# Kernel tuning notes

Measured on AMD Instinct MI355X. Metric: run time of the kernel, lower is better.

Reference implementation:

```python
import jax, jax.numpy as jnp
import numpy as np

NUM_USERS = 100000
NUM_ITEMS = 50000
N_NODES = NUM_USERS + NUM_ITEMS
N_EDGES = 2_000_000
D = 64          # embedding_dim
HEADS = 4
F1 = D // HEADS  # per-head out dim of gat1
BATCH = 16384
NEG_SLOPE = 0.2  # PyG GATConv default negative_slope


def setup_inputs() -> dict:
    key = jax.random.key(0)
    ks = jax.random.split(key, 13)
    inp = {}
    inp["edge_index"] = jax.random.randint(ks[0], (2, N_EDGES), 0, N_NODES, dtype=jnp.int64)
    inp["batch_user_idx"] = jax.random.randint(ks[1], (BATCH,), 0, NUM_USERS, dtype=jnp.int64)
    inp["batch_item_idx"] = jax.random.randint(ks[2], (BATCH,), 0, NUM_ITEMS, dtype=jnp.int64)
    # Embedding tables (nn.init.normal_ std=0.01)
    inp["user_emb"] = 0.01 * jax.random.normal(ks[3], (NUM_USERS, D), dtype=jnp.float32)
    inp["item_emb"] = 0.01 * jax.random.normal(ks[4], (NUM_ITEMS, D), dtype=jnp.float32)
    # gat1: GATConv(64, 16, heads=4, concat=True)
    inp["W1"] = jax.random.normal(ks[5], (D, HEADS * F1), dtype=jnp.float32) / np.sqrt(D)
    inp["a_src1"] = jax.random.normal(ks[6], (HEADS, F1), dtype=jnp.float32) / np.sqrt(F1)
    inp["a_dst1"] = jax.random.normal(ks[7], (HEADS, F1), dtype=jnp.float32) / np.sqrt(F1)
    inp["b1"] = jnp.zeros((HEADS * F1,), dtype=jnp.float32)
    # gat2: GATConv(64, 64, heads=1)
    inp["W2"] = jax.random.normal(ks[8], (D, D), dtype=jnp.float32) / np.sqrt(D)
    inp["a_src2"] = jax.random.normal(ks[9], (1, D), dtype=jnp.float32) / np.sqrt(D)
    inp["a_dst2"] = jax.random.normal(ks[10], (1, D), dtype=jnp.float32) / np.sqrt(D)
    inp["b2"] = jnp.zeros((D,), dtype=jnp.float32)
    return inp


def _gat_conv(x, src, dst, W, a_src, a_dst, b, num_nodes):
    """PyG GATConv (eval mode, concat, self-loops already in src/dst)."""
    H, F = a_src.shape
    h = (x @ W).reshape(num_nodes, H, F)                 # [N,H,F]
    alpha_s = jnp.einsum('nhf,hf->nh', h, a_src)         # [N,H]
    alpha_d = jnp.einsum('nhf,hf->nh', h, a_dst)
    e = alpha_s[src] + alpha_d[dst]                      # [E,H]
    e = jax.nn.leaky_relu(e, NEG_SLOPE)
    # scatter-softmax over destination neighborhoods
    m = jax.ops.segment_max(e, dst, num_segments=num_nodes)   # [N,H]
    e = jnp.exp(e - m[dst])
    denom = jax.ops.segment_sum(e, dst, num_segments=num_nodes)
    alpha = e / denom[dst]                               # [E,H]
    msg = h[src] * alpha[:, :, None]                     # [E,H,F]
    agg = jax.ops.segment_sum(msg, dst, num_segments=num_nodes)  # [N,H,F]
    return agg.reshape(num_nodes, H * F) + b


def reference(user_emb, item_emb, W1, a_src1, a_dst1, b1,
              W2, a_src2, a_dst2, b2,
              edge_index, batch_user_idx, batch_item_idx):
    x = jnp.concatenate([user_emb, item_emb], axis=0)    # [N,D]
    n = x.shape[0]
    loop = jnp.arange(n, dtype=edge_index.dtype)          # add_self_loops=True
    src = jnp.concatenate([edge_index[0], loop])
    dst = jnp.concatenate([edge_index[1], loop])
    x = jax.nn.elu(_gat_conv(x, src, dst, W1, a_src1, a_dst1, b1, n))
    x = jax.nn.elu(_gat_conv(x, src, dst, W2, a_src2, a_dst2, b2, n))
    u = x[batch_user_idx]
    v = x[batch_item_idx + NUM_USERS]
    return jax.nn.sigmoid(jnp.sum(u * v, axis=1))        # [BATCH]
```

## Files before the change

### kernel.cpp

```cpp
#include <hip/hip_runtime.h>
#include <math.h>

#define SHIFT 8
#define NBMAX 1024
#define CAP   4096
#define TILE  4096
#define HSCALE 64.0f

typedef float v2f __attribute__((ext_vector_type(2)));
typedef short bf16x8 __attribute__((ext_vector_type(8)));
typedef float f32x4 __attribute__((ext_vector_type(4)));

__device__ __forceinline__ unsigned short f2bf(float f) {
    unsigned u = __float_as_uint(f);
    unsigned r = u + 0x7FFFu + ((u >> 16) & 1u);
    return (unsigned short)(r >> 16);
}
__device__ __forceinline__ unsigned pack2bf(float lo, float hi) {
    return (unsigned)f2bf(lo) | ((unsigned)f2bf(hi) << 16);
}
__device__ __forceinline__ float bflo(unsigned u) { return __uint_as_float(u << 16); }
__device__ __forceinline__ float bfhi(unsigned u) { return __uint_as_float(u & 0xFFFF0000u); }


__global__ void k_prep_w(const float* __restrict__ W1, const float* __restrict__ W2,
                         unsigned short* __restrict__ WT1, unsigned short* __restrict__ WT2,
                         unsigned* __restrict__ gcur, int NB) {
    int t = blockIdx.x * 256 + threadIdx.x;
    if (t < 4096) {
        int n = t & 63, k = t >> 6;
        WT1[n * 64 + k] = f2bf(W1[k * 64 + n]);
        WT2[n * 64 + k] = f2bf(W2[k * 64 + n]);
    }
    if (t < NB) gcur[t] = (unsigned)t * CAP;
}


__global__ __launch_bounds__(512) void k_partition(
    const int* __restrict__ src, const int* __restrict__ dst, int E,
    unsigned* __restrict__ gcur, unsigned* __restrict__ pairs, int NB) {
    __shared__ unsigned lh[NBMAX];
    __shared__ unsigned lcur[NBMAX];
    int t = threadIdx.x;
    for (int q = t; q < NB; q += 512) lh[q] = 0;
    __syncthreads();
    int base = blockIdx.x * TILE;
    int end = min(E, base + TILE);
    for (int i = base + t; i < end; i += 512)
        atomicAdd(&lh[((unsigned)dst[i]) >> SHIFT], 1u);
    __syncthreads();
    for (int q = t; q < NB; q += 512) {
        unsigned c = lh[q];
        lcur[q] = c ? atomicAdd(&gcur[q], c) : 0u;
    }
    __syncthreads();
    for (int i = base + t; i < end; i += 512) {
        unsigned d = (unsigned)dst[i];
        unsigned pos = atomicAdd(&lcur[d >> SHIFT], 1u);
        pairs[pos] = ((d & 255u) << 18) | (unsigned)src[i];
    }
}

__global__ __launch_bounds__(512) void k_bucket_sort(
    const unsigned* __restrict__ pairs, const unsigned* __restrict__ gcur,
    unsigned* __restrict__ beg, unsigned* __restrict__ endd,
    int* __restrict__ srt, int N, int NB) {
    __shared__ unsigned lh[256];
    __shared__ unsigned lcur[256];
    __shared__ unsigned sh[256];
    __shared__ int ssrt[CAP];
    int b = blockIdx.x;
    int t = threadIdx.x;
    unsigned s0 = (unsigned)b * CAP;
    int cnt = (int)(gcur[b] - s0);
    if (t < 256) lh[t] = 0;
    __syncthreads();
    for (int i = t; i < cnt; i += 512)
        atomicAdd(&lh[pairs[s0 + i] >> 18], 1u);
    __syncthreads();
    unsigned deg_t = 0;
    if (t < 256) { deg_t = lh[t]; sh[t] = deg_t; }
    __syncthreads();
    for (int off = 1; off < 256; off <<= 1) {
        unsigned x = 0;
        if (t < 256 && t >= off) x = sh[t - off];
        __syncthreads();
        if (t < 256) sh[t] += x;
        __syncthreads();
    }
    if (t < 256) {
        unsigned excl = sh[t] - deg_t;
        lcur[t] = excl;
        int node = (b << SHIFT) + t;
        if (node < N) { beg[node] = s0 + excl; endd[node] = s0 + excl + deg_t; }
    }
    __syncthreads();
    for (int i = t; i < cnt; i += 512) {
        unsigned pk = pairs[s0 + i];
        unsigned p = atomicAdd(&lcur[pk >> 18], 1u);
        ssrt[p] = (int)(pk & 0x3FFFFu);
    }
    __syncthreads();
    for (int i = t; i < cnt; i += 512) srt[s0 + i] = ssrt[i];
}


template <int HT, int BIN>
__global__ __launch_bounds__(256) void k_linear_mfma(
    const void* __restrict__ xav, const void* __restrict__ xbv, int split,
    const unsigned short* __restrict__ WTg,
    const float* __restrict__ a_src, const float* __restrict__ a_dst,
    unsigned char* __restrict__ h, float* __restrict__ as_out,
    float* __restrict__ ad_out, int N) {
    __shared__ unsigned short sX[64 * 72];
    __shared__ unsigned short sWT[64 * 72];
    __shared__ float sH[64 * 68];
    int t = threadIdx.x;
    int nodeBase = blockIdx.x * 64;

    {
        int r = t >> 2, c4 = (t & 3) * 16;
        int n = nodeBase + r;
        uint4 A = {0,0,0,0}, Bv = {0,0,0,0};
        if (BIN) {
            if (n < N) {
                const unsigned short* row = (const unsigned short*)xav + (size_t)n * 64 + c4;
                A  = ((const uint4*)(const void*)row)[0];
                Bv = ((const uint4*)(const void*)row)[1];
            }
        } else {
            float4 v0 = {0,0,0,0}, v1 = {0,0,0,0}, v2 = {0,0,0,0}, v3 = {0,0,0,0};
            if (n < N) {
                const float* row = (n < split) ? ((const float*)xav + (size_t)n * 64 + c4)
                                               : ((const float*)xbv + (size_t)(n - split) * 64 + c4);
                const float4* r4 = (const float4*)row;
                v0 = r4[0]; v1 = r4[1]; v2 = r4[2]; v3 = r4[3];
            }
            A  = make_uint4(pack2bf(v0.x, v0.y), pack2bf(v0.z, v0.w),
                            pack2bf(v1.x, v1.y), pack2bf(v1.z, v1.w));
            Bv = make_uint4(pack2bf(v2.x, v2.y), pack2bf(v2.z, v2.w),
                            pack2bf(v3.x, v3.y), pack2bf(v3.z, v3.w));
        }
        *(uint4*)(void*)(sX + r * 72 + c4) = A;
        *(uint4*)(void*)(sX + r * 72 + c4 + 8) = Bv;
        const uint4* wsrc = (const uint4*)(const void*)WTg;
        int base = (r * 64 + c4) >> 3;
        *(uint4*)(void*)(sWT + r * 72 + c4) = wsrc[base];
        *(uint4*)(void*)(sWT + r * 72 + c4 + 8) = wsrc[base + 1];
    }
    __syncthreads();

    {
        int lane = t & 63, w = t >> 6;
        int gl = lane & 15, quad = lane >> 4;
        int m0 = w * 16;
        const bf16x8 a0 = *(const bf16x8*)(void*)(sX + (m0 + gl) * 72 + quad * 8);
        const bf16x8 a1 = *(const bf16x8*)(void*)(sX + (m0 + gl) * 72 + 32 + quad * 8);
        f32x4 acc[4];
#pragma unroll
        for (int tt = 0; tt < 4; ++tt) {
            const bf16x8 b0 = *(const bf16x8*)(void*)(sWT + (tt * 16 + gl) * 72 + quad * 8);
            const bf16x8 b1 = *(const bf16x8*)(void*)(sWT + (tt * 16 + gl) * 72 + 32 + quad * 8);
            f32x4 c = {0.f, 0.f, 0.f, 0.f};
            c = __builtin_amdgcn_mfma_f32_16x16x32_bf16(a0, b0, c, 0, 0, 0);
            c = __builtin_amdgcn_mfma_f32_16x16x32_bf16(a1, b1, c, 0, 0, 0);
            acc[tt] = c;
        }
#pragma unroll
        for (int tt = 0; tt < 4; ++tt)
#pragma unroll
            for (int rr = 0; rr < 4; ++rr)
                sH[(m0 + quad * 4 + rr) * 68 + tt * 16 + gl] = acc[tt][rr];
    }
    __syncthreads();

    {
        int m = t >> 2, p = t & 3;
        int n = nodeBase + m;
        const float4* sp = (const float4*)(void*)(sH + m * 68 + p * 16);
        float4 q0 = sp[0], q1 = sp[1], q2 = sp[2], q3 = sp[3];
        float hv[16] = {q0.x,q0.y,q0.z,q0.w, q1.x,q1.y,q1.z,q1.w,
                        q2.x,q2.y,q2.z,q2.w, q3.x,q3.y,q3.z,q3.w};
        if (n < N) {
            unsigned dwords[4];
#pragma unroll
            for (int q = 0; q < 4; ++q) {
                int d0 = __builtin_amdgcn_cvt_pk_fp8_f32(hv[4*q] * HSCALE, hv[4*q+1] * HSCALE, 0, false);
                d0 = __builtin_amdgcn_cvt_pk_fp8_f32(hv[4*q+2] * HSCALE, hv[4*q+3] * HSCALE, d0, true);
                dwords[q] = (unsigned)d0;
            }
            ((uint4*)h)[(size_t)n * 4 + p] = make_uint4(dwords[0], dwords[1], dwords[2], dwords[3]);
            float ps = 0.f, pd = 0.f;
#pragma unroll
            for (int i = 0; i < 16; ++i) {
                ps = fmaf(hv[i], a_src[p * 16 + i], ps);
                pd = fmaf(hv[i], a_dst[p * 16 + i], pd);
            }
            if (HT == 4) {
                as_out[n * 4 + p] = ps;
                ad_out[n * 4 + p] = pd;
            } else {
                ps += __shfl_xor(ps, 1, 64); ps += __shfl_xor(ps, 2, 64);
                pd += __shfl_xor(pd, 1, 64); pd += __shfl_xor(pd, 2, 64);
                if (p == 0) { as_out[n] = ps; ad_out[n] = pd; }
            }
        }
    }
}

template <int HT>
__global__ __launch_bounds__(256, 4) void k_gat(
                      const int* __restrict__ srt, const unsigned* __restrict__ beg,
                      const unsigned* __restrict__ endd,
                      const unsigned* __restrict__ hq, const float* __restrict__ as,
                      const float* __restrict__ ad, const float* __restrict__ b,
                      unsigned* __restrict__ xout, int N) {
    __shared__ unsigned s_vo[4][4][32];
    __shared__ float    s_w[4][4][HT * 32];

    int t = threadIdx.x;
    int lane = t & 63;
    int wv = t >> 6;
    int gl = lane & 15;
    int g  = lane >> 4;
    int wid = (int)((blockIdx.x * blockDim.x + t) >> 6);
    int d = wid * 4 + g;
    bool active = d < N;
    const int hh = (HT == 4) ? (gl >> 2) : 0;
    const unsigned gl4 = (unsigned)gl << 2;
    const char* hqb = (const char*)hq;
    const char* asb = (const char*)as;

    float adv = 0.f, l = 0.f;
    float a0 = 0.f, a1 = 0.f, a2 = 0.f, a3 = 0.f;
    int kb = 0, end = 0;
    if (active) {
        adv = ad[d * HT + hh];
        float e0 = as[d * HT + hh] + adv;
        e0 = (e0 > 0.f) ? e0 : 0.2f * e0;
        float w0 = __expf(e0);
        unsigned dw = hq[(size_t)d * 16 + gl];
        v2f lo = __builtin_amdgcn_cvt_pk_f32_fp8((int)dw, false);
        v2f hi = __builtin_amdgcn_cvt_pk_f32_fp8((int)dw, true);
        l = w0;
        a0 = w0 * lo.x; a1 = w0 * lo.y; a2 = w0 * hi.x; a3 = w0 * hi.y;
        kb = (int)beg[d];
        end = (int)endd[d];
    }

    int m = end - kb;
    while (__ballot(m > 0)) {
        unsigned v0 = 0, v1 = 0;
        if (gl < m)      v0 = ((unsigned)srt[kb + gl]) << 6;
        if (gl + 16 < m) v1 = ((unsigned)srt[kb + gl + 16]) << 6;

        float w0 = 0.f, w1 = 0.f;
        if (HT == 1) {
            float as0 = 0.f, as1 = 0.f;
            if (gl < m)      as0 = *(const float*)(asb + (v0 >> 4));
            if (gl + 16 < m) as1 = *(const float*)(asb + (v1 >> 4));
            s_vo[wv][g][gl]      = v0;
            s_vo[wv][g][gl + 16] = v1;
            asm volatile("s_waitcnt lgkmcnt(0)" ::: "memory");
            __builtin_amdgcn_sched_barrier(0);
            unsigned rr[32];
            const uint4* vob = (const uint4*)(const void*)&s_vo[wv][g][0];
#pragma unroll
            for (int c = 0; c < 8; ++c) {
                uint4 vv = vob[c];
                rr[4*c+0] = *(const unsigned*)(hqb + (vv.x + gl4));
                rr[4*c+1] = *(const unsigned*)(hqb + (vv.y + gl4));
                rr[4*c+2] = *(const unsigned*)(hqb + (vv.z + gl4));
                rr[4*c+3] = *(const unsigned*)(hqb + (vv.w + gl4));
            }
            if (gl < m) {
                float e = as0 + adv;
                e = (e > 0.f) ? e : 0.2f * e;
                w0 = __expf(e);
            }
            if (gl + 16 < m) {
                float e = as1 + adv;
                e = (e > 0.f) ? e : 0.2f * e;
                w1 = __expf(e);
            }
            s_w[wv][g][gl]      = w0;
            s_w[wv][g][gl + 16] = w1;
            asm volatile("s_waitcnt lgkmcnt(0)" ::: "memory");
            __builtin_amdgcn_sched_barrier(0);
            const float4* wrd = (const float4*)(const void*)&s_w[wv][g][0];
#pragma unroll
            for (int c = 0; c < 8; ++c) {
                float4 wc = wrd[c];
                float wj[4] = {wc.x, wc.y, wc.z, wc.w};
#pragma unroll
                for (int j = 0; j < 4; ++j) {
                    float w = wj[j];
                    unsigned rv = rr[4*c + j];
                    v2f lo = __builtin_amdgcn_cvt_pk_f32_fp8((int)rv, false);
                    v2f hi = __builtin_amdgcn_cvt_pk_f32_fp8((int)rv, true);
                    l += w;
                    a0 = fmaf(w, lo.x, a0);
                    a1 = fmaf(w, lo.y, a1);
                    a2 = fmaf(w, hi.x, a2);
                    a3 = fmaf(w, hi.y, a3);
                }
            }
        } else {
            s_vo[wv][g][gl]      = v0;
            s_vo[wv][g][gl + 16] = v1;
            asm volatile("s_waitcnt lgkmcnt(0)" ::: "memory");
            __builtin_amdgcn_sched_barrier(0);
            int eb = (gl & 3) << 3;
            const uint4* vop = (const uint4*)(const void*)&s_vo[wv][g][eb];
            uint4 va = vop[0], vb = vop[1];
            unsigned vs[8] = {va.x, va.y, va.z, va.w, vb.x, vb.y, vb.z, vb.w};
            float av[8];
#pragma unroll
            for (int r = 0; r < 8; ++r)
                av[r] = *(const float*)(asb + ((vs[r] >> 2) + ((unsigned)hh << 2)));
            unsigned rr[32];
            const uint4* vob = (const uint4*)(const void*)&s_vo[wv][g][0];
#pragma unroll
            for (int c = 0; c < 8; ++c) {
                uint4 vv = vob[c];
                rr[4*c+0] = *(const unsigned*)(hqb + (vv.x + gl4));
                rr[4*c+1] = *(const unsigned*)(hqb + (vv.y + gl4));
                rr[4*c+2] = *(const unsigned*)(hqb + (vv.z + gl4));
                rr[4*c+3] = *(const unsigned*)(hqb + (vv.w + gl4));
            }
            float wq[8];
#pragma unroll
            for (int r = 0; r < 8; ++r) {
                wq[r] = 0.f;
                if (eb + r < m) {
                    float e = av[r] + adv;
                    e = (e > 0.f) ? e : 0.2f * e;
                    wq[r] = __expf(e);
                }
            }
            float4* wp = (float4*)(void*)&s_w[wv][g][hh * 32 + eb];
            wp[0] = make_float4(wq[0], wq[1], wq[2], wq[3]);
            wp[1] = make_float4(wq[4], wq[5], wq[6], wq[7]);
            asm volatile("s_waitcnt lgkmcnt(0)" ::: "memory");
            __builtin_amdgcn_sched_barrier(0);
            const float4* wrd = (const float4*)(const void*)&s_w[wv][g][hh * 32];
#pragma unroll
            for (int c = 0; c < 8; ++c) {
                float4 wc = wrd[c];
                float wj[4] = {wc.x, wc.y, wc.z, wc.w};
#pragma unroll
                for (int j = 0; j < 4; ++j) {
                    float w = wj[j];
                    unsigned rv = rr[4*c + j];
                    v2f lo = __builtin_amdgcn_cvt_pk_f32_fp8((int)rv, false);
                    v2f hi = __builtin_amdgcn_cvt_pk_f32_fp8((int)rv, true);
                    l += w;
                    a0 = fmaf(w, lo.x, a0);
                    a1 = fmaf(w, lo.y, a1);
                    a2 = fmaf(w, hi.x, a2);
                    a3 = fmaf(w, hi.y, a3);
                }
            }
        }
        kb += 32;
        m = end - kb;
    }

    if (active) {
        float4 bb4 = ((const float4*)b)[gl];
        float rs = 1.f / (l * HSCALE);
        float v0 = a0 * rs + bb4.x;
        float v1 = a1 * rs + bb4.y;
        float v2 = a2 * rs + bb4.z;
        float v3 = a3 * rs + bb4.w;
        float o0 = (v0 > 0.f) ? v0 : expm1f(v0);
        float o1 = (v1 > 0.f) ? v1 : expm1f(v1);
        float o2 = (v2 > 0.f) ? v2 : expm1f(v2);
        float o3 = (v3 > 0.f) ? v3 : expm1f(v3);
        ((uint2*)xout)[(size_t)d * 16 + gl] = make_uint2(pack2bf(o0, o1), pack2bf(o2, o3));
    }
}

__global__ void k_dot_sig(const uint2* __restrict__ x2, const int* __restrict__ uidx,
                          const int* __restrict__ vidx, float* __restrict__ out,
                          int batch, int numUsers) {
    int lane = threadIdx.x & 63;
    int gl = lane & 15;
    int q = (int)(((blockIdx.x * blockDim.x + threadIdx.x) >> 6) * 4 + (lane >> 4));
    if (q >= batch) return;
    int u = uidx[q];
    int v = vidx[q] + numUsers;
    uint2 a = x2[(size_t)u * 16 + gl];
    uint2 c = x2[(size_t)v * 16 + gl];
    float p = bflo(a.x) * bflo(c.x) + bfhi(a.x) * bfhi(c.x)
            + bflo(a.y) * bflo(c.y) + bfhi(a.y) * bfhi(c.y);
#pragma unroll
    for (int off = 1; off < 16; off <<= 1) p += __shfl_xor(p, off, 64);
    if (gl == 0) out[q] = 1.f / (1.f + __expf(-p));
}


static inline int cdiv(long long a, long long b) { return (int)((a + b - 1) / b); }

extern "C" void kernel_launch(void* const* d_in, const int* in_sizes, int n_in,
                              void* d_out, int out_size, void* d_ws, size_t ws_size,
                              hipStream_t stream) {
    const int* edge_index = (const int*)d_in[0];
    const int* buidx      = (const int*)d_in[1];
    const int* biidx      = (const int*)d_in[2];
    const float* user_emb = (const float*)d_in[3];
    const float* item_emb = (const float*)d_in[4];
    const float* W1     = (const float*)d_in[5];
    const float* a_src1 = (const float*)d_in[6];
    const float* a_dst1 = (const float*)d_in[7];
    const float* b1     = (const float*)d_in[8];
    const float* W2     = (const float*)d_in[9];
    const float* a_src2 = (const float*)d_in[10];
    const float* a_dst2 = (const float*)d_in[11];
    const float* b2     = (const float*)d_in[12];
    float* out = (float*)d_out;

    const int E  = in_sizes[0] / 2;
    const int B  = in_sizes[1];
    const int NU = in_sizes[3] / 64;
    const int NI = in_sizes[4] / 64;
    const int N  = NU + NI;
    const int NB = cdiv(N, 1 << SHIFT);

    const int* src = edge_index;
    const int* dst = edge_index + E;

    float* ws = (float*)d_ws;
    size_t off = 0;
    unsigned* x_buf  = (unsigned*)(ws + off); off += (size_t)N * 32;
    unsigned* h_buf  = (unsigned*)(ws + off); off += (size_t)N * 16;
    float*    as_b   = ws + off; off += (size_t)N * 4;
    float*    ad_b   = ws + off; off += (size_t)N * 4;
    unsigned* gcur_b = (unsigned*)(ws + off); off += NBMAX;
    unsigned* beg_b  = (unsigned*)(ws + off); off += (size_t)N;
    unsigned* end_b  = (unsigned*)(ws + off); off += (size_t)N;
    unsigned* pairs_b= (unsigned*)(ws + off); off += (size_t)NB * CAP;
    int*      srt_b  = (int*)(ws + off); off += (size_t)NB * CAP;
    unsigned short* wt1_b = (unsigned short*)(ws + off); off += 2048;
    unsigned short* wt2_b = (unsigned short*)(ws + off); off += 2048;

    const int BS = 256;

    k_prep_w<<<16, BS, 0, stream>>>(W1, W2, wt1_b, wt2_b, gcur_b, NB);
    k_partition<<<cdiv(E, TILE), 512, 0, stream>>>(src, dst, E, gcur_b, pairs_b, NB);
    k_bucket_sort<<<NB, 512, 0, stream>>>(pairs_b, gcur_b, beg_b, end_b, srt_b, N, NB);

    k_linear_mfma<4, 0><<<cdiv(N, 64), BS, 0, stream>>>(user_emb, item_emb, NU, wt1_b,
                                                        a_src1, a_dst1,
                                                        (unsigned char*)h_buf, as_b, ad_b, N);
    k_gat<4><<<cdiv((long long)N * 16, BS), BS, 0, stream>>>(
        srt_b, beg_b, end_b, h_buf, as_b, ad_b, b1, x_buf, N);

    k_linear_mfma<1, 1><<<cdiv(N, 64), BS, 0, stream>>>(x_buf, x_buf, N, wt2_b,
                                                        a_src2, a_dst2,
                                                        (unsigned char*)h_buf, as_b, ad_b, N);
    k_gat<1><<<cdiv((long long)N * 16, BS), BS, 0, stream>>>(
        srt_b, beg_b, end_b, h_buf, as_b, ad_b, b2, x_buf, N);

    k_dot_sig<<<cdiv((long long)B * 16, BS), BS, 0, stream>>>(
        (const uint2*)x_buf, buidx, biidx, out, B, NU);
}
```

Baseline: 255.4 us.

## Sort destination nodes by degree and shrink GAT edge chunk to 16

Adds a degree histogram, a scan and a scatter pass that build a permutation of destination nodes grouped by in-degree (capped at 255). Both GAT kernels process nodes in that order, so the four 16-lane groups in a wavefront have similar edge counts and the __ballot loop wastes fewer iterations. The per-iteration edge chunk drops from 32 to 16, which lowers register and LDS use and padding waste for low-degree nodes but doubles the loop trips for high-degree ones. It costs three extra small kernel launches and an indirect perm load, and output writes become scattered.

```diff
diff --git a/kernel.cpp b/kernel.cpp
--- a/kernel.cpp
+++ b/kernel.cpp
@@ -25,7 +25,7 @@
 
 __global__ void k_prep_w(const float* __restrict__ W1, const float* __restrict__ W2,
                          unsigned short* __restrict__ WT1, unsigned short* __restrict__ WT2,
-                         unsigned* __restrict__ gcur, int NB) {
+                         unsigned* __restrict__ gcur, unsigned* __restrict__ hist, int NB) {
     int t = blockIdx.x * 256 + threadIdx.x;
     if (t < 4096) {
         int n = t & 63, k = t >> 6;
@@ -33,6 +33,7 @@
         WT2[n * 64 + k] = f2bf(W2[k * 64 + n]);
     }
     if (t < NB) gcur[t] = (unsigned)t * CAP;
+    if (t < 256) hist[t] = 0;
 }
 
 
@@ -105,6 +106,49 @@
 }
 
 
+__global__ __launch_bounds__(256) void k_deg_hist(
+    const unsigned* __restrict__ beg, const unsigned* __restrict__ endd,
+    int N, unsigned* __restrict__ hist) {
+    __shared__ unsigned lh[256];
+    int t = threadIdx.x;
+    lh[t] = 0;
+    __syncthreads();
+    for (int i = blockIdx.x * 256 + t; i < N; i += gridDim.x * 256) {
+        int dg = min((int)(endd[i] - beg[i]), 255);
+        atomicAdd(&lh[dg], 1u);
+    }
+    __syncthreads();
+    if (lh[t]) atomicAdd(&hist[t], lh[t]);
+}
+
+__global__ __launch_bounds__(256) void k_deg_scan(unsigned* __restrict__ hist) {
+    __shared__ unsigned sh[256];
+    int t = threadIdx.x;
+    unsigned v = hist[t];
+    sh[t] = v;
+    __syncthreads();
+    for (int off = 1; off < 256; off <<= 1) {
+        unsigned x = 0;
+        if (t >= off) x = sh[t - off];
+        __syncthreads();
+        sh[t] += x;
+        __syncthreads();
+    }
+    hist[t] = sh[t] - v;
+}
+
+__global__ __launch_bounds__(256) void k_deg_scatter(
+    const unsigned* __restrict__ beg, const unsigned* __restrict__ endd,
+    int N, unsigned* __restrict__ offs, int* __restrict__ perm) {
+    int i = blockIdx.x * 256 + threadIdx.x;
+    if (i < N) {
+        int dg = min((int)(endd[i] - beg[i]), 255);
+        unsigned p = atomicAdd(&offs[dg], 1u);
+        perm[p] = i;
+    }
+}
+
+
 template <int HT, int BIN>
 __global__ __launch_bounds__(256) void k_linear_mfma(
     const void* __restrict__ xav, const void* __restrict__ xbv, int split,
@@ -210,13 +254,14 @@
 
 template <int HT>
 __global__ __launch_bounds__(256, 4) void k_gat(
+                      const int* __restrict__ perm,
                       const int* __restrict__ srt, const unsigned* __restrict__ beg,
                       const unsigned* __restrict__ endd,
                       const unsigned* __restrict__ hq, const float* __restrict__ as,
                       const float* __restrict__ ad, const float* __restrict__ b,
                       unsigned* __restrict__ xout, int N) {
-    __shared__ unsigned s_vo[4][4][32];
-    __shared__ float    s_w[4][4][HT * 32];
+    __shared__ unsigned s_vo[4][4][24];
+    __shared__ float    s_w[4][4][(HT == 4) ? 80 : 24];
 
     int t = threadIdx.x;
     int lane = t & 63;
@@ -224,8 +269,9 @@
     int gl = lane & 15;
     int g  = lane >> 4;
     int wid = (int)((blockIdx.x * blockDim.x + t) >> 6);
-    int d = wid * 4 + g;
-    bool active = d < N;
+    int dp = wid * 4 + g;
+    bool active = dp < N;
+    int d = active ? perm[dp] : 0;
     const int hh = (HT == 4) ? (gl >> 2) : 0;
     const unsigned gl4 = (unsigned)gl << 2;
     const char* hqb = (const char*)hq;
@@ -250,46 +296,37 @@
 
     int m = end - kb;
     while (__ballot(m > 0)) {
-        unsigned v0 = 0, v1 = 0;
-        if (gl < m)      v0 = ((unsigned)srt[kb + gl]) << 6;
-        if (gl + 16 < m) v1 = ((unsigned)srt[kb + gl + 16]) << 6;
-
-        float w0 = 0.f, w1 = 0.f;
+        unsigned v0 = 0;
+        if (gl < m) v0 = ((unsigned)srt[kb + gl]) << 6;
+
         if (HT == 1) {
-            float as0 = 0.f, as1 = 0.f;
-            if (gl < m)      as0 = *(const float*)(asb + (v0 >> 4));
-            if (gl + 16 < m) as1 = *(const float*)(asb + (v1 >> 4));
-            s_vo[wv][g][gl]      = v0;
-            s_vo[wv][g][gl + 16] = v1;
+            float as0 = 0.f;
+            if (gl < m) as0 = *(const float*)(asb + (v0 >> 4));
+            s_vo[wv][g][gl] = v0;
             asm volatile("s_waitcnt lgkmcnt(0)" ::: "memory");
             __builtin_amdgcn_sched_barrier(0);
-            unsigned rr[32];
+            unsigned rr[16];
             const uint4* vob = (const uint4*)(const void*)&s_vo[wv][g][0];
 #pragma unroll
-            for (int c = 0; c < 8; ++c) {
+            for (int c = 0; c < 4; ++c) {
                 uint4 vv = vob[c];
                 rr[4*c+0] = *(const unsigned*)(hqb + (vv.x + gl4));
                 rr[4*c+1] = *(const unsigned*)(hqb + (vv.y + gl4));
                 rr[4*c+2] = *(const unsigned*)(hqb + (vv.z + gl4));
                 rr[4*c+3] = *(const unsigned*)(hqb + (vv.w + gl4));
             }
+            float w0 = 0.f;
             if (gl < m) {
                 float e = as0 + adv;
                 e = (e > 0.f) ? e : 0.2f * e;
                 w0 = __expf(e);
             }
-            if (gl + 16 < m) {
-                float e = as1 + adv;
-                e = (e > 0.f) ? e : 0.2f * e;
-                w1 = __expf(e);
-            }
-            s_w[wv][g][gl]      = w0;
-            s_w[wv][g][gl + 16] = w1;
+            s_w[wv][g][gl] = w0;
             asm volatile("s_waitcnt lgkmcnt(0)" ::: "memory");
             __builtin_amdgcn_sched_barrier(0);
             const float4* wrd = (const float4*)(const void*)&s_w[wv][g][0];
 #pragma unroll
-            for (int c = 0; c < 8; ++c) {
+            for (int c = 0; c < 4; ++c) {
                 float4 wc = wrd[c];
                 float wj[4] = {wc.x, wc.y, wc.z, wc.w};
 #pragma unroll
@@ -306,31 +343,30 @@
                 }
             }
         } else {
-            s_vo[wv][g][gl]      = v0;
-            s_vo[wv][g][gl + 16] = v1;
+            s_vo[wv][g][gl] = v0;
             asm volatile("s_waitcnt lgkmcnt(0)" ::: "memory");
             __builtin_amdgcn_sched_barrier(0);
-            int eb = (gl & 3) << 3;
+            int eb = (gl & 3) << 2;
             const uint4* vop = (const uint4*)(const void*)&s_vo[wv][g][eb];
-            uint4 va = vop[0], vb = vop[1];
-            unsigned vs[8] = {va.x, va.y, va.z, va.w, vb.x, vb.y, vb.z, vb.w};
-            float av[8];
-#pragma unroll
-            for (int r = 0; r < 8; ++r)
+            uint4 va = vop[0];
+            unsigned vs[4] = {va.x, va.y, va.z, va.w};
+            float av[4];
+#pragma unroll
+            for (int r = 0; r < 4; ++r)
                 av[r] = *(const float*)(asb + ((vs[r] >> 2) + ((unsigned)hh << 2)));
-            unsigned rr[32];
+            unsigned rr[16];
             const uint4* vob = (const uint4*)(const void*)&s_vo[wv][g][0];
 #pragma unroll
-            for (int c = 0; c < 8; ++c) {
+            for (int c = 0; c < 4; ++c) {
                 uint4 vv = vob[c];
                 rr[4*c+0] = *(const unsigned*)(hqb + (vv.x + gl4));
                 rr[4*c+1] = *(const unsigned*)(hqb + (vv.y + gl4));
                 rr[4*c+2] = *(const unsigned*)(hqb + (vv.z + gl4));
                 rr[4*c+3] = *(const unsigned*)(hqb + (vv.w + gl4));
             }
-            float wq[8];
-#pragma unroll
-            for (int r = 0; r < 8; ++r) {
+            float wq[4];
+#pragma unroll
+            for (int r = 0; r < 4; ++r) {
                 wq[r] = 0.f;
                 if (eb + r < m) {
                     float e = av[r] + adv;
@@ -338,14 +374,13 @@
                     wq[r] = __expf(e);
                 }
             }
-            float4* wp = (float4*)(void*)&s_w[wv][g][hh * 32 + eb];
+            float4* wp = (float4*)(void*)&s_w[wv][g][hh * 20 + eb];
             wp[0] = make_float4(wq[0], wq[1], wq[2], wq[3]);
-            wp[1] = make_float4(wq[4], wq[5], wq[6], wq[7]);
             asm volatile("s_waitcnt lgkmcnt(0)" ::: "memory");
             __builtin_amdgcn_sched_barrier(0);
-            const float4* wrd = (const float4*)(const void*)&s_w[wv][g][hh * 32];
-#pragma unroll
-            for (int c = 0; c < 8; ++c) {
+            const float4* wrd = (const float4*)(const void*)&s_w[wv][g][hh * 20];
+#pragma unroll
+            for (int c = 0; c < 4; ++c) {
                 float4 wc = wrd[c];
                 float wj[4] = {wc.x, wc.y, wc.z, wc.w};
 #pragma unroll
@@ -362,7 +397,7 @@
                 }
             }
         }
-        kb += 32;
+        kb += 16;
         m = end - kb;
     }
 
@@ -443,24 +478,30 @@
     int*      srt_b  = (int*)(ws + off); off += (size_t)NB * CAP;
     unsigned short* wt1_b = (unsigned short*)(ws + off); off += 2048;
     unsigned short* wt2_b = (unsigned short*)(ws + off); off += 2048;
+    unsigned* hist_b = (unsigned*)(ws + off); off += 256;
+    int*      perm_b = (int*)(ws + off); off += (size_t)N;
 
     const int BS = 256;
 
-    k_prep_w<<<16, BS, 0, stream>>>(W1, W2, wt1_b, wt2_b, gcur_b, NB);
+    k_prep_w<<<16, BS, 0, stream>>>(W1, W2, wt1_b, wt2_b, gcur_b, hist_b, NB);
     k_partition<<<cdiv(E, TILE), 512, 0, stream>>>(src, dst, E, gcur_b, pairs_b, NB);
     k_bucket_sort<<<NB, 512, 0, stream>>>(pairs_b, gcur_b, beg_b, end_b, srt_b, N, NB);
+
+    k_deg_hist<<<128, BS, 0, stream>>>(beg_b, end_b, N, hist_b);
+    k_deg_scan<<<1, BS, 0, stream>>>(hist_b);
+    k_deg_scatter<<<cdiv(N, BS), BS, 0, stream>>>(beg_b, end_b, N, hist_b, perm_b);
 
     k_linear_mfma<4, 0><<<cdiv(N, 64), BS, 0, stream>>>(user_emb, item_emb, NU, wt1_b,
                                                         a_src1, a_dst1,
                                                         (unsigned char*)h_buf, as_b, ad_b, N);
     k_gat<4><<<cdiv((long long)N * 16, BS), BS, 0, stream>>>(
-        srt_b, beg_b, end_b, h_buf, as_b, ad_b, b1, x_buf, N);
+        perm_b, srt_b, beg_b, end_b, h_buf, as_b, ad_b, b1, x_buf, N);
 
     k_linear_mfma<1, 1><<<cdiv(N, 64), BS, 0, stream>>>(x_buf, x_buf, N, wt2_b,
                                                         a_src2, a_dst2,
                                                         (unsigned char*)h_buf, as_b, ad_b, N);
     k_gat<1><<<cdiv((long long)N * 16, BS), BS, 0, stream>>>(
-        srt_b, beg_b, end_b, h_buf, as_b, ad_b, b2, x_buf, N);
+        perm_b, srt_b, beg_b, end_b, h_buf, as_b, ad_b, b2, x_buf, N);
 
     k_dot_sig<<<cdiv((long long)B * 16, BS), BS, 0, stream>>>(
         (const uint2*)x_buf, buidx, biidx, out, B, NU);
```

Result: slower. 732.8 us (+186.9%).
